# Optimization experiments

Measured on AMD Instinct MI355X. Metric: run time of the kernel, lower is better.

Reference implementation:

```python
import jax, jax.numpy as jnp
import numpy as np

D_MODEL = 1024
N_HEADS = 16
HEAD_DIM = D_MODEL // N_HEADS
ROPE_BASE = 10000.0


def rope_rot(t, pos):
    # t: [B, L, H, hd], pos: [L] int32 absolute positions. Rotate-half RoPE.
    hd = t.shape[-1]
    inv_freq = 1.0 / (ROPE_BASE ** (jnp.arange(0, hd, 2, dtype=jnp.float32) / hd))
    freqs = pos.astype(jnp.float32)[:, None] * inv_freq[None, :]  # [L, hd/2]
    cos = jnp.cos(freqs)[None, :, None, :]  # [1, L, 1, hd/2]
    sin = jnp.sin(freqs)[None, :, None, :]
    t1, t2 = t[..., : hd // 2], t[..., hd // 2 :]
    return jnp.concatenate([t1 * cos - t2 * sin, t2 * cos + t1 * sin], axis=-1)


def setup_inputs() -> dict:
    key = jax.random.key(0)
    ks = jax.random.split(key, 8)
    B, L, S = 8, 16, 8192
    x = jax.random.normal(ks[0], (B, L, D_MODEL), dtype=jnp.float32)
    cache_k = jax.random.normal(ks[1], (B, S, N_HEADS, HEAD_DIM), dtype=jnp.float32)
    cache_v = jax.random.normal(ks[2], (B, S, N_HEADS, HEAD_DIM), dtype=jnp.float32)
    sc = 1.0 / np.sqrt(D_MODEL)
    qkv_w = jax.random.normal(ks[3], (D_MODEL, 3 * D_MODEL), dtype=jnp.float32) * sc
    qkv_b = jnp.zeros((3 * D_MODEL,), dtype=jnp.float32)
    o_w = jax.random.normal(ks[4], (D_MODEL, D_MODEL), dtype=jnp.float32) * sc
    o_b = jnp.zeros((D_MODEL,), dtype=jnp.float32)
    return {
        "x": x,
        "cache_k": cache_k,
        "cache_v": cache_v,
        "qkv_w": qkv_w,
        "qkv_b": qkv_b,
        "o_w": o_w,
        "o_b": o_b,
        "cache_index": S,
    }


def reference(x, cache_k, cache_v, qkv_w, qkv_b, o_w, o_b, cache_index):
    B, L, _ = x.shape
    qkv = x @ qkv_w + qkv_b  # [B, L, 3*d]
    q, k, v = jnp.split(qkv, 3, axis=-1)
    q = q.reshape(B, L, N_HEADS, HEAD_DIM)
    k = k.reshape(B, L, N_HEADS, HEAD_DIM)
    v = v.reshape(B, L, N_HEADS, HEAD_DIM)
    pos = cache_index + jnp.arange(L, dtype=jnp.int32)
    q = rope_rot(q, pos)
    k = rope_rot(k, pos)
    # streaming: append new k/v to cache (cached entries already RoPE-rotated)
    k_full = jnp.concatenate([cache_k, k], axis=1)  # [B, S+L, H, hd]
    v_full = jnp.concatenate([cache_v, v], axis=1)
    scale = 1.0 / jnp.sqrt(jnp.asarray(HEAD_DIM, dtype=q.dtype))
    scores = jnp.einsum("blhd,bshd->bhls", q, k_full) * scale  # [B, H, L, S+L]
    probs = jax.nn.softmax(scores, axis=-1)  # no mask in original module
    out = jnp.einsum("bhls,bshd->blhd", probs, v_full)
    out = out.reshape(B, L, D_MODEL)
    return out @ o_w + o_b
```

## Files before the change

kernel.cpp:

```cpp
#include <hip/hip_runtime.h>

#define B_ 8
#define L_ 16
#define H_ 16
#define D_ 64
#define DM 1024
#define S_ 8192

__device__ __forceinline__ void gld_lds16(const float* g, float* l) {
  __builtin_amdgcn_global_load_lds(
      (const __attribute__((address_space(1))) void*)g,
      (__attribute__((address_space(3))) void*)l, 16, 0, 0);
}

__global__ void __launch_bounds__(256) gemm_splitk_kernel(
    const float* __restrict__ A, const float* __restrict__ W,
    float* __restrict__ part, int lda, int ldw, int Kchunk)
{
  const int c0 = blockIdx.x * 64;
  const int k0 = blockIdx.y * Kchunk;
  const int t  = threadIdx.x;
  __shared__ float xs[32][132];
  __shared__ float wsm[32][64];
  float acc[8][4];
  #pragma unroll
  for (int i = 0; i < 8; ++i)
    #pragma unroll
    for (int j = 0; j < 4; ++j) acc[i][j] = 0.f;
  const int rg = t >> 4, cg = t & 15;
  const int r0 = rg * 8, ct0 = cg * 4;
  for (int ks = 0; ks < Kchunk; ks += 32) {
    __syncthreads();
    #pragma unroll
    for (int i = 0; i < 4; ++i) {
      int fi = t + i * 256;
      int r = fi >> 3, kq = fi & 7;
      float4 v = *(const float4*)(A + (size_t)r * lda + k0 + ks + kq * 4);
      xs[kq*4+0][r] = v.x; xs[kq*4+1][r] = v.y;
      xs[kq*4+2][r] = v.z; xs[kq*4+3][r] = v.w;
    }
    #pragma unroll
    for (int i = 0; i < 2; ++i) {
      int si = t + i * 256;
      int kk = si >> 4, cq = si & 15;
      *(float4*)&wsm[kk][cq*4] =
          *(const float4*)(W + (size_t)(k0 + ks + kk) * ldw + c0 + cq * 4);
    }
    __syncthreads();
    #pragma unroll
    for (int kk = 0; kk < 32; ++kk) {
      float a[8], bb[4];
      *(float4*)&a[0] = *(const float4*)&xs[kk][r0];
      *(float4*)&a[4] = *(const float4*)&xs[kk][r0 + 4];
      *(float4*)&bb[0] = *(const float4*)&wsm[kk][ct0];
      #pragma unroll
      for (int ii = 0; ii < 8; ++ii)
        #pragma unroll
        for (int jj = 0; jj < 4; ++jj)
          acc[ii][jj] = fmaf(a[ii], bb[jj], acc[ii][jj]);
    }
  }
  float* po = part + (size_t)blockIdx.y * 128 * ldw;
  #pragma unroll
  for (int ii = 0; ii < 8; ++ii)
    #pragma unroll
    for (int jj = 0; jj < 4; ++jj)
      po[(size_t)(r0 + ii) * ldw + c0 + ct0 + jj] = acc[ii][jj];
}

__global__ void ropefuse_kernel(const float* __restrict__ part,
                                const float* __restrict__ bias,
                                const int* __restrict__ cidx,
                                float* __restrict__ qh, float* __restrict__ kn,
                                float* __restrict__ vn)
{
  int gt = blockIdx.x * 256 + threadIdx.x;
  int i = gt & 31, l = (gt >> 5) & 15, h = (gt >> 9) & 15, b = gt >> 13;
  int row = b * L_ + l;
  const int PS = 128 * 3072;
  const float* pr = part + (size_t)row * 3072;
  int cq = h * 64 + i;
  int cols[6] = {cq, cq + 32, 1024 + cq, 1024 + cq + 32, 2048 + cq, 2048 + cq + 32};
  float v[6];
  #pragma unroll
  for (int c = 0; c < 6; ++c) {
    float s = bias[cols[c]];
    #pragma unroll
    for (int ks = 0; ks < 4; ++ks) s += pr[(size_t)ks * PS + cols[c]];
    v[c] = s;
  }
  int pos = cidx[0] + l;
  float inv = exp2f((float)i * (-13.287712379549449f / 32.0f));
  float fr = (float)pos * inv;
  float sn, cs;
  sincosf(fr, &sn, &cs);
  int ob = ((b * H_ + h) * L_ + l) * 64;
  qh[ob + i]      = (v[0] * cs - v[1] * sn) * 0.125f;
  qh[ob + 32 + i] = (v[1] * cs + v[0] * sn) * 0.125f;
  kn[ob + i]      = v[2] * cs - v[3] * sn;
  kn[ob + 32 + i] = v[3] * cs + v[2] * sn;
  vn[ob + i]      = v[4];
  vn[ob + 32 + i] = v[5];
}

__global__ void __launch_bounds__(512, 4) attn_partial_kernel(
    const float* __restrict__ qh, const float* __restrict__ kc,
    const float* __restrict__ vc, float* __restrict__ opart,
    float* __restrict__ lpart)
{
  const int chunk = blockIdx.x;
  const int b     = blockIdx.y;
  const int tid   = threadIdx.x;
  const int w = tid >> 6, lane = tid & 63;
  const int h = tid >> 5, dh = tid & 1;
  const int l = (tid >> 1) & 15;
  __shared__ float kv[4 * 4096];

  float4 qr[8];
  {
    const float* qb = qh + (size_t)b * 16384 + (size_t)tid * 32;
    #pragma unroll
    for (int j = 0; j < 8; ++j)
      qr[j] = *(const float4*)(qb + ((j ^ (dh << 2)) << 2));
  }
  float4 o[8];
  #pragma unroll
  for (int j = 0; j < 8; ++j) o[j].x = o[j].y = o[j].z = o[j].w = 0.f;
  float l_run = 0.f;

  const size_t kbase = (size_t)b * S_ * DM;
  const int st0 = chunk * 128;

  const float* wsrc0 = (w < 4 ? kc : vc) + kbase + (size_t)(w & 3) * 512 + lane * 4;
  float* wdst0 = &kv[0] + (w < 4 ? 0 : 2048) + (w & 3) * 512;
  auto issue = [&](int T) {
    const float* src = wsrc0 + (size_t)(st0 + T * 2) * DM;
    float* dst = wdst0 + (T & 3) * 4096;
    gld_lds16(src, dst);
    gld_lds16(src + 256, dst + 256);
  };

  issue(0); issue(1); issue(2);

  const int koff = h * 64 + dh * 32;
#define STEP(T, WAITOP) do {                                                  \
    asm volatile(WAITOP ::: "memory");                                        \
    __builtin_amdgcn_sched_barrier(0);                                        \
    __builtin_amdgcn_s_barrier();                                             \
    if ((T) + 3 < 64) issue((T) + 3);                                         \
    const float* sb = &kv[((T) & 3) * 4096];                                  \
    _Pragma("unroll")                                                         \
    for (int r = 0; r < 2; ++r) {                                             \
      const float* kr = sb + r * 1024 + koff;                                 \
      const float* vr = sb + 2048 + r * 1024 + koff;                          \
      float sc = 0.f;                                                         \
      _Pragma("unroll")                                                       \
      for (int j = 0; j < 8; ++j) {                                           \
        float4 k4 = *(const float4*)(kr + ((j ^ (dh << 2)) << 2));            \
        sc += k4.x * qr[j].x + k4.y * qr[j].y + k4.z * qr[j].z + k4.w * qr[j].w;\
      }                                                                       \
      float s = sc + __shfl_xor(sc, 1);                                       \
      float pex = __expf(s);                                                  \
      l_run += pex;                                                           \
      _Pragma("unroll")                                                       \
      for (int j = 0; j < 8; ++j) {                                           \
        float4 v4 = *(const float4*)(vr + ((j ^ (dh << 2)) << 2));            \
        o[j].x = fmaf(pex, v4.x, o[j].x);                                     \
        o[j].y = fmaf(pex, v4.y, o[j].y);                                     \
        o[j].z = fmaf(pex, v4.z, o[j].z);                                     \
        o[j].w = fmaf(pex, v4.w, o[j].w);                                     \
      }                                                                       \
    } } while (0)

  for (int t = 0; t < 62; ++t) STEP(t, "s_waitcnt vmcnt(4)");
  STEP(62, "s_waitcnt vmcnt(2)");
  STEP(63, "s_waitcnt vmcnt(0)");
#undef STEP

  const size_t ob = (((size_t)(b * 64 + chunk) * 16 + h) * 16 + l) * 64;
  #pragma unroll
  for (int j = 0; j < 8; ++j)
    *(float4*)&opart[ob + dh * 32 + ((j ^ (dh << 2)) << 2)] = o[j];
  if (dh == 0)
    lpart[((b * 64 + chunk) * 16 + h) * 16 + l] = l_run;
}

__global__ void __launch_bounds__(64) combine_kernel(
    const float* __restrict__ qh, const float* __restrict__ kn,
    const float* __restrict__ vn, const float* __restrict__ opart,
    const float* __restrict__ lpart, float* __restrict__ attn)
{
  const int bh = blockIdx.x;
  const int b = bh >> 4, h = bh & 15;
  const int l0 = blockIdx.y * 4;
  const int lane = threadIdx.x;
  __shared__ float kb[1024], vb[1024], qb[256];
  __shared__ float scn[4][16];
  for (int i = 0; i < 16; ++i) {
    kb[i * 64 + lane] = kn[(size_t)(bh * 16 + i) * 64 + lane];
    vb[i * 64 + lane] = vn[(size_t)(bh * 16 + i) * 64 + lane];
  }
  {
    int ll = lane >> 4, sl = lane & 15;
    *(float4*)&qb[ll * 64 + sl * 4] =
        *(const float4*)&qh[(size_t)(bh * 16 + l0 + ll) * 64 + sl * 4];
  }
  __syncthreads();
  {
    int ll = lane >> 4, sp = lane & 15;
    float a = 0.f;
    for (int d = 0; d < 64; ++d) a += qb[ll * 64 + d] * kb[sp * 64 + d];
    scn[ll][sp] = a;
  }
  __syncthreads();
  for (int ll = 0; ll < 4; ++ll) {
    const int l = l0 + ll;
    float den = 0.f, od = 0.f;
    for (int c = 0; c < 64; ++c) {
      den += lpart[((b * 64 + c) * 16 + h) * 16 + l];
      od  += opart[(((size_t)(b * 64 + c) * 16 + h) * 16 + l) * 64 + lane];
    }
    #pragma unroll
    for (int sp = 0; sp < 16; ++sp) {
      float pex = __expf(scn[ll][sp]);
      den += pex;
      od += pex * vb[sp * 64 + lane];
    }
    attn[((size_t)(b * 16 + l) * 16 + h) * 64 + lane] = od / den;
  }
}

__global__ void reduce_out_kernel(const float* __restrict__ part2,
                                  const float* __restrict__ ob,
                                  float* __restrict__ out)
{
  int idx = blockIdx.x * 256 + threadIdx.x;
  int c = idx & 1023;
  float s = ob[c];
  #pragma unroll
  for (int ks = 0; ks < 8; ++ks) s += part2[(size_t)ks * 131072 + idx];
  out[idx] = s;
}

extern "C" void kernel_launch(void* const* d_in, const int* in_sizes, int n_in,
                              void* d_out, int out_size, void* d_ws, size_t ws_size,
                              hipStream_t stream) {
  (void)in_sizes; (void)n_in; (void)out_size; (void)ws_size;
  const float* x       = (const float*)d_in[0];
  const float* cache_k = (const float*)d_in[1];
  const float* cache_v = (const float*)d_in[2];
  const float* qkv_w   = (const float*)d_in[3];
  const float* qkv_b   = (const float*)d_in[4];
  const float* o_w     = (const float*)d_in[5];
  const float* o_b     = (const float*)d_in[6];
  const int*   cidx    = (const int*)d_in[7];
  float* out = (float*)d_out;

  float* ws    = (float*)d_ws;
  float* big   = ws;
  float* part1 = big;
  float* opart = big;
  float* part2 = big;
  float* qh    = big + 8388608;
  float* kn    = qh + 131072;
  float* vn    = kn + 131072;
  float* lpart = vn + 131072;
  float* attn  = lpart + 131072;

  gemm_splitk_kernel<<<dim3(48, 4), 256, 0, stream>>>(x, qkv_w, part1, 1024, 3072, 256);
  ropefuse_kernel<<<256, 256, 0, stream>>>(part1, qkv_b, cidx, qh, kn, vn);
  attn_partial_kernel<<<dim3(64, 8), 512, 0, stream>>>(qh, cache_k, cache_v,
                                                       opart, lpart);
  combine_kernel<<<dim3(128, 4), 64, 0, stream>>>(qh, kn, vn, opart, lpart, attn);
  gemm_splitk_kernel<<<dim3(16, 8), 256, 0, stream>>>(attn, o_w, part2, 1024, 1024, 128);
  reduce_out_kernel<<<512, 256, 0, stream>>>(part2, o_b, out);
}
```

Before: 208.9 us.

## Remap attention threads to 4 queries x 8 dims and reduce with DPP

The partial attention kernel now gives each thread 4 query rows and an 8-wide slice of head dimension instead of 1 query and 32 dims. Each K/V element loaded from LDS is reused across 4 queries, which cuts LDS read traffic per FMA. The score reduction across the 8 dim-lanes uses DPP row shifts plus one shuffle, and the LDS staging layout is interleaved to match. The trade-off is more cross-lane reduction work and more exp calls per thread, and the DPP lane pattern has to line up exactly with the dq mapping for the scores to be correct.

```diff
diff --git a/kernel.cpp b/kernel.cpp
--- a/kernel.cpp
+++ b/kernel.cpp
@@ -11,6 +11,12 @@
   __builtin_amdgcn_global_load_lds(
       (const __attribute__((address_space(1))) void*)g,
       (__attribute__((address_space(3))) void*)l, 16, 0, 0);
+}
+
+template <int CTRL>
+__device__ __forceinline__ float add_dpp(float x) {
+  int y = __builtin_amdgcn_update_dpp(0, __float_as_int(x), CTRL, 0xf, 0xf, false);
+  return x + __int_as_float(y);
 }
 
 __global__ void __launch_bounds__(256) gemm_splitk_kernel(
@@ -112,63 +118,73 @@
   const int b     = blockIdx.y;
   const int tid   = threadIdx.x;
   const int w = tid >> 6, lane = tid & 63;
-  const int h = tid >> 5, dh = tid & 1;
-  const int l = (tid >> 1) & 15;
+  const int h = tid >> 5, dq = (tid >> 2) & 7, lg = tid & 3;
   __shared__ float kv[4 * 4096];
 
-  float4 qr[8];
+  float4 q0[4], q1[4], o0[4], o1[4];
   {
-    const float* qb = qh + (size_t)b * 16384 + (size_t)tid * 32;
-    #pragma unroll
-    for (int j = 0; j < 8; ++j)
-      qr[j] = *(const float4*)(qb + ((j ^ (dh << 2)) << 2));
-  }
-  float4 o[8];
-  #pragma unroll
-  for (int j = 0; j < 8; ++j) o[j].x = o[j].y = o[j].z = o[j].w = 0.f;
-  float l_run = 0.f;
+    const float* qb = qh + ((size_t)b * 256 + h * 16 + lg * 4) * 64 + dq * 8;
+    #pragma unroll
+    for (int li = 0; li < 4; ++li) {
+      q0[li] = *(const float4*)(qb + li * 64);
+      q1[li] = *(const float4*)(qb + li * 64 + 4);
+      o0[li].x = o0[li].y = o0[li].z = o0[li].w = 0.f;
+      o1[li].x = o1[li].y = o1[li].z = o1[li].w = 0.f;
+    }
+  }
+  float l_run[4] = {0.f, 0.f, 0.f, 0.f};
 
   const size_t kbase = (size_t)b * S_ * DM;
   const int st0 = chunk * 128;
-
-  const float* wsrc0 = (w < 4 ? kc : vc) + kbase + (size_t)(w & 3) * 512 + lane * 4;
-  float* wdst0 = &kv[0] + (w < 4 ? 0 : 2048) + (w & 3) * 512;
+  const int rS = (w >> 1) & 1, sub = w & 1;
+  const float* stream = (w < 4) ? kc : vc;
+  const int srcoff = 8 * lane + 4 * sub;
+
   auto issue = [&](int T) {
-    const float* src = wsrc0 + (size_t)(st0 + T * 2) * DM;
-    float* dst = wdst0 + (T & 3) * 4096;
-    gld_lds16(src, dst);
-    gld_lds16(src + 256, dst + 256);
+    const float* rowp = stream + kbase + (size_t)(st0 + T * 2 + rS) * DM + srcoff;
+    float* dst = &kv[(T & 3) * 4096 + w * 512];
+    gld_lds16(rowp, dst);
+    gld_lds16(rowp + 512, dst + 256);
   };
 
   issue(0); issue(1); issue(2);
 
-  const int koff = h * 64 + dh * 32;
+  const int g4 = 4 * (h * 8 + dq);
+
 #define STEP(T, WAITOP) do {                                                  \
     asm volatile(WAITOP ::: "memory");                                        \
     __builtin_amdgcn_sched_barrier(0);                                        \
     __builtin_amdgcn_s_barrier();                                             \
     if ((T) + 3 < 64) issue((T) + 3);                                         \
-    const float* sb = &kv[((T) & 3) * 4096];                                  \
+    const float* u = &kv[((T) & 3) * 4096];                                   \
     _Pragma("unroll")                                                         \
     for (int r = 0; r < 2; ++r) {                                             \
-      const float* kr = sb + r * 1024 + koff;                                 \
-      const float* vr = sb + 2048 + r * 1024 + koff;                          \
-      float sc = 0.f;                                                         \
+      const float* kp = u + r * 1024 + g4;                                    \
+      float4 ka  = *(const float4*)kp;                                        \
+      float4 kb2 = *(const float4*)(kp + 512);                                \
+      float4 va  = *(const float4*)(kp + 2048);                               \
+      float4 vb2 = *(const float4*)(kp + 2560);                               \
+      float pex[4];                                                           \
       _Pragma("unroll")                                                       \
-      for (int j = 0; j < 8; ++j) {                                           \
-        float4 k4 = *(const float4*)(kr + ((j ^ (dh << 2)) << 2));            \
-        sc += k4.x * qr[j].x + k4.y * qr[j].y + k4.z * qr[j].z + k4.w * qr[j].w;\
+      for (int li = 0; li < 4; ++li) {                                        \
+        float sc = ka.x*q0[li].x + ka.y*q0[li].y + ka.z*q0[li].z + ka.w*q0[li].w \
+                 + kb2.x*q1[li].x + kb2.y*q1[li].y + kb2.z*q1[li].z + kb2.w*q1[li].w; \
+        sc = add_dpp<0x124>(sc);           \
+        sc = add_dpp<0x128>(sc);           \
+        sc += __shfl_xor(sc, 16);        \
+        pex[li] = __expf(sc);                                                 \
+        l_run[li] += pex[li];                                                 \
       }                                                                       \
-      float s = sc + __shfl_xor(sc, 1);                                       \
-      float pex = __expf(s);                                                  \
-      l_run += pex;                                                           \
       _Pragma("unroll")                                                       \
-      for (int j = 0; j < 8; ++j) {                                           \
-        float4 v4 = *(const float4*)(vr + ((j ^ (dh << 2)) << 2));            \
-        o[j].x = fmaf(pex, v4.x, o[j].x);                                     \
-        o[j].y = fmaf(pex, v4.y, o[j].y);                                     \
-        o[j].z = fmaf(pex, v4.z, o[j].z);                                     \
-        o[j].w = fmaf(pex, v4.w, o[j].w);                                     \
+      for (int li = 0; li < 4; ++li) {                                        \
+        o0[li].x = fmaf(pex[li], va.x,  o0[li].x);                            \
+        o0[li].y = fmaf(pex[li], va.y,  o0[li].y);                            \
+        o0[li].z = fmaf(pex[li], va.z,  o0[li].z);                            \
+        o0[li].w = fmaf(pex[li], va.w,  o0[li].w);                            \
+        o1[li].x = fmaf(pex[li], vb2.x, o1[li].x);                            \
+        o1[li].y = fmaf(pex[li], vb2.y, o1[li].y);                            \
+        o1[li].z = fmaf(pex[li], vb2.z, o1[li].z);                            \
+        o1[li].w = fmaf(pex[li], vb2.w, o1[li].w);                            \
       }                                                                       \
     } } while (0)
 
@@ -177,12 +193,17 @@
   STEP(63, "s_waitcnt vmcnt(0)");
 #undef STEP
 
-  const size_t ob = (((size_t)(b * 64 + chunk) * 16 + h) * 16 + l) * 64;
-  #pragma unroll
-  for (int j = 0; j < 8; ++j)
-    *(float4*)&opart[ob + dh * 32 + ((j ^ (dh << 2)) << 2)] = o[j];
-  if (dh == 0)
-    lpart[((b * 64 + chunk) * 16 + h) * 16 + l] = l_run;
+  const size_t ob = (((size_t)(b * 64 + chunk) * 16 + h) * 16 + lg * 4) * 64 + dq * 8;
+  #pragma unroll
+  for (int li = 0; li < 4; ++li) {
+    *(float4*)&opart[ob + (size_t)li * 64]     = o0[li];
+    *(float4*)&opart[ob + (size_t)li * 64 + 4] = o1[li];
+  }
+  if (dq == 0) {
+    #pragma unroll
+    for (int li = 0; li < 4; ++li)
+      lpart[((b * 64 + chunk) * 16 + h) * 16 + lg * 4 + li] = l_run[li];
+  }
 }
 
 __global__ void __launch_bounds__(64) combine_kernel(
```

After: 224.0 us. 7.3% more time.
